# Optimization experiments

Measured on AMD Instinct MI355X. Metric: run time of the kernel, lower is better.

## Reference

```python
import jax, jax.numpy as jnp
import numpy as np

N = 8192      # atoms
B = 64        # molecules
E = 262144    # edges
S = 4         # species
NMAX = 8      # radial basis size
CUT = 5.0     # cutoff radius
AVG_ATOMS = 128.0
E_SCALE = 1.0
PS_DIM = (S * NMAX) ** 2 * 4  # l_max=3 -> 4 l channels -> 4096
H1, H2 = 1024, 1024
OUT = 1


def _sph_harm(u):
    # real spherical harmonics up to l=3, input unit vectors [E,3] -> [E,16]
    x, y, z = u[:, 0], u[:, 1], u[:, 2]
    x2, y2, z2 = x * x, y * y, z * z
    return jnp.stack([
        0.28209479 * jnp.ones_like(x),
        0.48860251 * y, 0.48860251 * z, 0.48860251 * x,
        1.09254843 * x * y, 1.09254843 * y * z, 0.31539157 * (3.0 * z2 - 1.0),
        1.09254843 * x * z, 0.54627422 * (x2 - y2),
        0.59004359 * y * (3.0 * x2 - y2), 2.89061144 * x * y * z,
        0.45704579 * y * (5.0 * z2 - 1.0), 0.37317633 * z * (5.0 * z2 - 3.0),
        0.45704579 * x * (5.0 * z2 - 1.0), 1.44530572 * z * (x2 - y2),
        0.59004359 * x * (x2 - 3.0 * y2),
    ], axis=-1)


def setup_inputs() -> dict:
    key = jax.random.key(0)
    ks = jax.random.split(key, 12)
    positions = jax.random.normal(ks[0], (N, 3), dtype=jnp.float32) * 1.5  # dense cloud so many pairs < CUT
    cells = jnp.tile(20.0 * jnp.eye(3, dtype=jnp.float32)[None], (B, 1, 1))
    numbers = jax.random.randint(ks[1], (N,), 0, S)
    edge_indices = jax.random.randint(ks[2], (2, E), 0, N)
    edge_offsets = jnp.zeros((E, 3), dtype=jnp.float32)
    batch = jnp.arange(N) // (N // B)
    gamma = 1.0 + 0.1 * jax.random.normal(ks[3], (PS_DIM,), dtype=jnp.float32)
    beta = 0.1 * jax.random.normal(ks[4], (PS_DIM,), dtype=jnp.float32)
    W_ps = jax.random.normal(ks[5], (PS_DIM, OUT), dtype=jnp.float32) / np.sqrt(PS_DIM)
    W1 = jax.random.normal(ks[6], (PS_DIM, H1), dtype=jnp.float32) / np.sqrt(PS_DIM)
    W2 = jax.random.normal(ks[7], (H1, H2), dtype=jnp.float32) / np.sqrt(H1)
    W3 = jax.random.normal(ks[8], (H2, OUT), dtype=jnp.float32) / np.sqrt(H2)
    W_comp = jax.random.normal(ks[9], (S, OUT), dtype=jnp.float32) / np.sqrt(S)
    return dict(positions=positions, cells=cells, numbers=numbers,
                edge_indices=edge_indices, edge_offsets=edge_offsets, batch=batch,
                gamma=gamma, beta=beta, W_ps=W_ps, W1=W1, W2=W2, W3=W3, W_comp=W_comp)


def reference(positions, cells, numbers, edge_indices, edge_offsets, batch,
              gamma, beta, W_ps, W1, W2, W3, W_comp):
    i, j = edge_indices[0], edge_indices[1]  # center, neighbor
    # periodic shift: fractional offsets through the cell of the center's molecule
    shift = jnp.einsum('ec,ecd->ed', edge_offsets, cells[batch[i]])
    rvec = positions[j] - positions[i] + shift                      # [E,3]
    r = jnp.sqrt(jnp.sum(rvec * rvec, axis=-1) + 1e-12)             # [E]
    u = rvec / r[:, None]
    fc = 0.5 * (jnp.cos(jnp.pi * jnp.minimum(r, CUT) / CUT) + 1.0) * (r < CUT)
    n = jnp.arange(1, NMAX + 1, dtype=positions.dtype)
    R = fc[:, None] * jnp.sin(jnp.pi * n[None, :] * r[:, None] / CUT) / r[:, None]  # [E,NMAX]
    Y = _sph_harm(u)                                                # [E,16]
    edge_feat = R[:, :, None] * Y[:, None, :]                       # [E,NMAX,16]
    # spherical expansion c[i, species(j), n, lm] via scatter-add
    seg = i * S + numbers[j]
    c = jax.ops.segment_sum(edge_feat, seg, num_segments=N * S)     # [N*S,NMAX,16]
    c = c.reshape(N, S * NMAX, 16)
    # power spectrum: contract over m within each l block
    bounds = [(0, 1), (1, 4), (4, 9), (9, 16)]
    p = [jnp.einsum('ixm,iym->ixy', c[:, :, s:e], c[:, :, s:e]) for s, e in bounds]
    ps = jnp.stack(p, axis=-1).reshape(N, PS_DIM)                   # [N,4096]
    # LayerNorm (eps=1e-5, affine)
    mu = jnp.mean(ps, axis=-1, keepdims=True)
    var = jnp.var(ps, axis=-1, keepdims=True)
    psn = (ps - mu) / jnp.sqrt(var + 1e-5) * gamma + beta
    # linear branch + MLP branch
    psl = psn @ W_ps                                                # [N,1]
    h = jax.nn.silu(psn @ W1)
    h = jax.nn.silu(h @ W2)
    psnn = h @ W3                                                   # [N,1]
    # pool atomic energies into per-molecule totals (index_add)
    energies = jax.ops.segment_sum(psl + psnn, batch, num_segments=B) / AVG_ATOMS
    # eval path: composition baseline
    comp = jax.ops.segment_sum(jax.nn.one_hot(numbers, S, dtype=psn.dtype), batch, num_segments=B)
    return energies * E_SCALE + comp @ W_comp                       # [B,1]
```

## Files before the change

### kernel.cpp

```cpp
#include <hip/hip_runtime.h>
#include <hip/hip_bf16.h>
#include <math.h>

#define N_ATOMS 8192
#define B_BATCH 64
#define E_EDGES 262144
#define S_SPEC 4
#define NMAX 8
#define PS_DIM 4096
#define H1_DIM 1024
#define CAP4 48
#define CUTR 5.0f
#define PI_F 3.14159265358979f

typedef __bf16 bf16;
typedef bf16 bf16x8 __attribute__((ext_vector_type(8)));
typedef float floatx4 __attribute__((ext_vector_type(4)));
typedef int intx8 __attribute__((ext_vector_type(8)));
typedef unsigned char u8;

__device__ __forceinline__ void g2lds16(const void* g, void* l) {
    __builtin_amdgcn_global_load_lds(
        (const __attribute__((address_space(1))) void*)g,
        (__attribute__((address_space(3))) void*)l, 16, 0, 0);
}

__device__ __forceinline__ int pk_fp8x4(float a, float b, float c, float d) {
    int lo = __builtin_amdgcn_cvt_pk_fp8_f32(a, b, 0, false);
    return __builtin_amdgcn_cvt_pk_fp8_f32(c, d, lo, true);
}

__global__ __launch_bounds__(256) void scatter_kernel(
    const float* __restrict__ pos, const float* __restrict__ cells,
    const int* __restrict__ numbers, const int* __restrict__ ei,
    const float* __restrict__ eo, const int* __restrict__ batch,
    int* __restrict__ cnt, float4* __restrict__ bucket)
{
    int e = blockIdx.x * 256 + threadIdx.x;
    int i = ei[e];
    int j = ei[E_EDGES + e];
    int b = batch[i];
    const float* cell = cells + b * 9;
    float o0 = eo[e * 3 + 0], o1 = eo[e * 3 + 1], o2 = eo[e * 3 + 2];
    float rv[3];
    #pragma unroll
    for (int d = 0; d < 3; ++d) {
        float shift = o0 * cell[0 * 3 + d] + o1 * cell[1 * 3 + d] + o2 * cell[2 * 3 + d];
        rv[d] = pos[j * 3 + d] - pos[i * 3 + d] + shift;
    }
    float r2 = rv[0] * rv[0] + rv[1] * rv[1] + rv[2] * rv[2] + 1e-12f;
    if (r2 >= CUTR * CUTR) return;
    float r = sqrtf(r2);
    float a1 = r * (PI_F / CUTR);
    int sp = numbers[j];
    int q = i * S_SPEC + sp;
    int slot = atomicAdd(&cnt[q], 1);
    if (slot < CAP4)
        bucket[q * CAP4 + slot] = make_float4(rv[0], rv[1], rv[2], a1);
}

__global__ __launch_bounds__(256) void transpose_convert2(
    const float* __restrict__ W1, u8* __restrict__ Wt1,
    const float* __restrict__ W2, u8* __restrict__ Wt2)
{
    const float* W; u8* Wt; int K; float scale; int bx;
    if (blockIdx.x < 128) { W = W1; Wt = Wt1; K = PS_DIM; scale = 64.0f; bx = blockIdx.x; }
    else                  { W = W2; Wt = Wt2; K = H1_DIM; scale = 32.0f; bx = blockIdx.x - 128; }
    const int Nc = H1_DIM;
    __shared__ float t[32][33];
    int k0 = bx * 32, n0 = blockIdx.y * 32;
    int tx = threadIdx.x & 31, ty = threadIdx.x >> 5;
    #pragma unroll
    for (int r = 0; r < 32; r += 8)
        t[ty + r][tx] = W[(size_t)(k0 + ty + r) * Nc + n0 + tx];
    __syncthreads();
    if (threadIdx.x < 64) {
        int nl = threadIdx.x >> 1, cc = threadIdx.x & 1;
        int n = n0 + nl;
        unsigned int w[4];
        #pragma unroll
        for (int g = 0; g < 4; ++g) {
            int kb = cc * 16 + g * 4;
            w[g] = (unsigned int)pk_fp8x4(
                t[kb + 0][nl] * scale, t[kb + 1][nl] * scale,
                t[kb + 2][nl] * scale, t[kb + 3][nl] * scale);
        }
        int gc = (k0 >> 4) + cc;
        int gcs = (gc & ~7) | ((gc & 7) ^ (n & 7));
        *(uint4*)(Wt + (size_t)n * K + (size_t)gcs * 16) = make_uint4(w[0], w[1], w[2], w[3]);
    }
}

__global__ __launch_bounds__(256) void accum_ps_kernel(
    const float4* __restrict__ bucket, const int* __restrict__ cnt,
    const float* __restrict__ gamma, const float* __restrict__ beta,
    const float* __restrict__ Wps, u8* __restrict__ psn, float* __restrict__ psl)
{
    __shared__ __align__(16) float cl[4][32 * 20];
    __shared__ __align__(16) u8 ps_s8[PS_DIM];
    __shared__ float red[8];
    __shared__ float red2[4];

    int t = threadIdx.x;
    int wv = t >> 6, lane = t & 63;
    int atom0 = blockIdx.x * 4;

    {
        int atom = atom0 + wv;
        int sp_l = lane >> 4;
        int nidx = (lane >> 1) & 7;
        float nf = (float)(nidx + 1);
        int par = lane & 1;

        int myCnt = cnt[atom * S_SPEC + sp_l];
        if (myCnt > CAP4) myCnt = CAP4;
        int m1 = max(myCnt, __shfl_xor(myCnt, 16));
        int mx = max(m1, __shfl_xor(m1, 32));

        const float4* q = bucket + (size_t)(atom * S_SPEC + sp_l) * CAP4;
        float acc[8] = {};
        #pragma unroll 2
        for (int e = 0; e < mx; ++e) {
            float4 d = q[e];
            bool valid = e < myCnt;
            float a1 = d.w;
            float inv_r = (PI_F / CUTR) * __frcp_rn(a1);
            float fc = 0.5f * __cosf(a1) + 0.5f;
            float rn = fc * inv_r * __sinf(nf * a1);
            rn = valid ? rn : 0.0f;

            float x = d.x * inv_r, y = d.y * inv_r, z = d.z * inv_r;
            float x2 = x * x, y2 = y * y, z2 = z * z;
            float Ys[8];
            if (par == 0) {
                Ys[0] = 0.28209479f;
                Ys[1] = 0.48860251f * y;
                Ys[2] = 0.48860251f * z;
                Ys[3] = 0.48860251f * x;
                Ys[4] = 1.09254843f * x * y;
                Ys[5] = 1.09254843f * y * z;
                Ys[6] = 0.31539157f * (3.0f * z2 - 1.0f);
                Ys[7] = 1.09254843f * x * z;
            } else {
                Ys[0] = 0.54627422f * (x2 - y2);
                Ys[1] = 0.59004359f * y * (3.0f * x2 - y2);
                Ys[2] = 2.89061144f * x * y * z;
                Ys[3] = 0.45704579f * y * (5.0f * z2 - 1.0f);
                Ys[4] = 0.37317633f * z * (5.0f * z2 - 3.0f);
                Ys[5] = 0.45704579f * x * (5.0f * z2 - 1.0f);
                Ys[6] = 1.44530572f * z * (x2 - y2);
                Ys[7] = 0.59004359f * x * (x2 - 3.0f * y2);
            }
            #pragma unroll
            for (int k = 0; k < 8; ++k) acc[k] += rn * Ys[k];
        }
        int X = sp_l * 8 + nidx;
        float* dst = &cl[wv][X * 20 + par * 8];
        *(float4*)(dst + 0) = make_float4(acc[0], acc[1], acc[2], acc[3]);
        *(float4*)(dst + 4) = make_float4(acc[4], acc[5], acc[6], acc[7]);
    }
    __syncthreads();

    for (int a = 0; a < 4; ++a) {
        int atom = atom0 + a;
        const float* cl_x = cl[a];

        int y = t & 31;
        int xb = t >> 5;
        float4 cya = *(const float4*)&cl_x[y * 20 + 0];
        float4 cyb = *(const float4*)&cl_x[y * 20 + 4];
        float4 cyc = *(const float4*)&cl_x[y * 20 + 8];
        float4 cyd = *(const float4*)&cl_x[y * 20 + 12];

        float ps[4][4];
        float sum = 0.0f, sumsq = 0.0f;
        #pragma unroll
        for (int q = 0; q < 4; ++q) {
            int x = xb + 8 * q;
            float4 xa = *(const float4*)&cl_x[x * 20 + 0];
            float4 xbv = *(const float4*)&cl_x[x * 20 + 4];
            float4 xc = *(const float4*)&cl_x[x * 20 + 8];
            float4 xd = *(const float4*)&cl_x[x * 20 + 12];
            float s0 = xa.x * cya.x;
            float s1 = xa.y * cya.y + xa.z * cya.z + xa.w * cya.w;
            float s2 = xbv.x * cyb.x + xbv.y * cyb.y + xbv.z * cyb.z + xbv.w * cyb.w
                     + xc.x * cyc.x;
            float s3 = xc.y * cyc.y + xc.z * cyc.z + xc.w * cyc.w
                     + xd.x * cyd.x + xd.y * cyd.y + xd.z * cyd.z + xd.w * cyd.w;
            ps[q][0] = s0; ps[q][1] = s1; ps[q][2] = s2; ps[q][3] = s3;
            sum += s0 + s1 + s2 + s3;
            sumsq += s0 * s0 + s1 * s1 + s2 * s2 + s3 * s3;
        }
        #pragma unroll
        for (int o = 32; o > 0; o >>= 1) {
            sum += __shfl_down(sum, o);
            sumsq += __shfl_down(sumsq, o);
        }
        if ((t & 63) == 0) { red[wv] = sum; red[4 + wv] = sumsq; }
        __syncthreads();
        float tot = red[0] + red[1] + red[2] + red[3];
        float totsq = red[4] + red[5] + red[6] + red[7];
        float mu = tot * (1.0f / PS_DIM);
        float var = totsq * (1.0f / PS_DIM) - mu * mu;
        float inv = rsqrtf(var + 1e-5f);

        float pacc = 0.0f;
        #pragma unroll
        for (int q = 0; q < 4; ++q) {
            int p = t + 256 * q;
            float4 g = *(const float4*)(gamma + p * 4);
            float4 bt = *(const float4*)(beta + p * 4);
            float4 w = *(const float4*)(Wps + p * 4);
            float v0 = (ps[q][0] - mu) * inv * g.x + bt.x;
            float v1 = (ps[q][1] - mu) * inv * g.y + bt.y;
            float v2 = (ps[q][2] - mu) * inv * g.z + bt.z;
            float v3 = (ps[q][3] - mu) * inv * g.w + bt.w;
            pacc += v0 * w.x + v1 * w.y + v2 * w.z + v3 * w.w;
            ((int*)ps_s8)[p] = pk_fp8x4(v0, v1, v2, v3);
        }
        __syncthreads();
        u8* rowp = psn + (size_t)atom * PS_DIM;
        int key = atom & 7;
        int gcs = (t & ~7) | ((t & 7) ^ key);
        *(uint4*)(rowp + (size_t)gcs * 16) = *(const uint4*)(ps_s8 + (size_t)t * 16);

        #pragma unroll
        for (int o = 32; o > 0; o >>= 1) pacc += __shfl_down(pacc, o);
        if ((t & 63) == 0) red2[wv] = pacc;
        __syncthreads();
        if (t == 0) psl[atom] = red2[0] + red2[1] + red2[2] + red2[3];
    }
}

__global__ __launch_bounds__(256) void gemm_f8_kernel(
    const u8* __restrict__ A, const u8* __restrict__ Bt,
    u8* __restrict__ H, int M, int Nc, int K, float invs)
{
    __shared__ __align__(16) char smem[65536];
    int tid = threadIdx.x;
    int bm = blockIdx.x, bn = blockIdx.y;
    int wave = tid >> 6, lane = tid & 63;
    int wm = (wave >> 1) * 64, wn = (wave & 1) * 64;
    int lm = lane & 15, quad = lane >> 4;

    floatx4 acc[4][4] = {};
    const int rowA0 = bm * 128, rowB0 = bn * 128;
    const size_t stride = (size_t)K;
    const char* Ab = (const char*)A + (size_t)rowA0 * stride;
    const char* Bb = (const char*)Bt + (size_t)rowB0 * stride;
    const int sA = 0x7F7F7F7F, sB = 0x7F7F7F7F;

    for (int k0 = 0; k0 < K; k0 += 256) {
        #pragma unroll
        for (int s = 0; s < 8; ++s) {
            int L = s * 256 + tid;
            int row = L >> 4, boff = (L & 15) * 16;
            int lbase = (s * 256 + wave * 64) * 16;
            g2lds16(Ab + (size_t)row * stride + k0 + boff, smem + lbase);
        }
        #pragma unroll
        for (int s = 0; s < 8; ++s) {
            int L = s * 256 + tid;
            int row = L >> 4, boff = (L & 15) * 16;
            int lbase = (s * 256 + wave * 64) * 16;
            g2lds16(Bb + (size_t)row * stride + k0 + boff, smem + 32768 + lbase);
        }
        __syncthreads();
        int key = lm & 7;
        int c0 = (2 * quad) ^ key, c1 = (2 * quad + 1) ^ key;
        #pragma unroll
        for (int h = 0; h < 2; ++h) {
            intx8 af[4], bfr[4];
            #pragma unroll
            for (int mi = 0; mi < 4; ++mi) {
                const char* base = smem + (wm + mi * 16 + lm) * 256 + h * 128;
                uint4 lo = *(const uint4*)(base + c0 * 16);
                uint4 hi = *(const uint4*)(base + c1 * 16);
                af[mi][0] = lo.x; af[mi][1] = lo.y; af[mi][2] = lo.z; af[mi][3] = lo.w;
                af[mi][4] = hi.x; af[mi][5] = hi.y; af[mi][6] = hi.z; af[mi][7] = hi.w;
            }
            #pragma unroll
            for (int ni = 0; ni < 4; ++ni) {
                const char* base = smem + 32768 + (wn + ni * 16 + lm) * 256 + h * 128;
                uint4 lo = *(const uint4*)(base + c0 * 16);
                uint4 hi = *(const uint4*)(base + c1 * 16);
                bfr[ni][0] = lo.x; bfr[ni][1] = lo.y; bfr[ni][2] = lo.z; bfr[ni][3] = lo.w;
                bfr[ni][4] = hi.x; bfr[ni][5] = hi.y; bfr[ni][6] = hi.z; bfr[ni][7] = hi.w;
            }
            #pragma unroll
            for (int mi = 0; mi < 4; ++mi)
                #pragma unroll
                for (int ni = 0; ni < 4; ++ni)
                    acc[mi][ni] = __builtin_amdgcn_mfma_scale_f32_16x16x128_f8f6f4(
                        af[mi], bfr[ni], acc[mi][ni], 0, 0, 0, sA, 0, sB);
        }
        __syncthreads();
    }

    u8* Cs8 = (u8*)smem;
    #pragma unroll
    for (int mi = 0; mi < 4; ++mi)
        #pragma unroll
        for (int ni = 0; ni < 4; ++ni)
            #pragma unroll
            for (int r = 0; r < 4; ++r) {
                int row = wm + mi * 16 + quad * 4 + r;
                int col = wn + ni * 16 + lm;
                float v = acc[mi][ni][r] * invs;
                v = v / (1.0f + __expf(-v));
                int pk = __builtin_amdgcn_cvt_pk_fp8_f32(v, 0.0f, 0, false);
                Cs8[row * 128 + col] = (u8)(pk & 0xFF);
            }
    __syncthreads();
    #pragma unroll
    for (int c2 = 0; c2 < 4; ++c2) {
        int L = c2 * 256 + tid;
        int row = L >> 3, cc = L & 7;
        int gcs = cc ^ (row & 7);
        *(uint4*)(H + (size_t)(rowA0 + row) * Nc + (size_t)(bn * 8 + gcs) * 16) =
            *(const uint4*)(Cs8 + (size_t)L * 16);
    }
}

__global__ __launch_bounds__(256) void gemm2_fused_kernel(
    const u8* __restrict__ A, const u8* __restrict__ Bt,
    const float* __restrict__ W3, float* __restrict__ nn_part,
    int Nc, int K, float invs)
{
    __shared__ __align__(16) char smem[65536];
    int tid = threadIdx.x;
    int bm = blockIdx.x, bn = blockIdx.y;
    int wave = tid >> 6, lane = tid & 63;
    int wm = (wave >> 1) * 64, wn = (wave & 1) * 64;
    int lm = lane & 15, quad = lane >> 4;

    floatx4 acc[4][4] = {};
    const int rowA0 = bm * 128, rowB0 = bn * 128;
    const size_t stride = (size_t)K;
    const char* Ab = (const char*)A + (size_t)rowA0 * stride;
    const char* Bb = (const char*)Bt + (size_t)rowB0 * stride;
    const int sA = 0x7F7F7F7F, sB = 0x7F7F7F7F;

    for (int k0 = 0; k0 < K; k0 += 256) {
        #pragma unroll
        for (int s = 0; s < 8; ++s) {
            int L = s * 256 + tid;
            int row = L >> 4, boff = (L & 15) * 16;
            int lbase = (s * 256 + wave * 64) * 16;
            g2lds16(Ab + (size_t)row * stride + k0 + boff, smem + lbase);
        }
        #pragma unroll
        for (int s = 0; s < 8; ++s) {
            int L = s * 256 + tid;
            int row = L >> 4, boff = (L & 15) * 16;
            int lbase = (s * 256 + wave * 64) * 16;
            g2lds16(Bb + (size_t)row * stride + k0 + boff, smem + 32768 + lbase);
        }
        __syncthreads();
        int key = lm & 7;
        int c0 = (2 * quad) ^ key, c1 = (2 * quad + 1) ^ key;
        #pragma unroll
        for (int h = 0; h < 2; ++h) {
            intx8 af[4], bfr[4];
            #pragma unroll
            for (int mi = 0; mi < 4; ++mi) {
                const char* base = smem + (wm + mi * 16 + lm) * 256 + h * 128;
                uint4 lo = *(const uint4*)(base + c0 * 16);
                uint4 hi = *(const uint4*)(base + c1 * 16);
                af[mi][0] = lo.x; af[mi][1] = lo.y; af[mi][2] = lo.z; af[mi][3] = lo.w;
                af[mi][4] = hi.x; af[mi][5] = hi.y; af[mi][6] = hi.z; af[mi][7] = hi.w;
            }
            #pragma unroll
            for (int ni = 0; ni < 4; ++ni) {
                const char* base = smem + 32768 + (wn + ni * 16 + lm) * 256 + h * 128;
                uint4 lo = *(const uint4*)(base + c0 * 16);
                uint4 hi = *(const uint4*)(base + c1 * 16);
                bfr[ni][0] = lo.x; bfr[ni][1] = lo.y; bfr[ni][2] = lo.z; bfr[ni][3] = lo.w;
                bfr[ni][4] = hi.x; bfr[ni][5] = hi.y; bfr[ni][6] = hi.z; bfr[ni][7] = hi.w;
            }
            #pragma unroll
            for (int mi = 0; mi < 4; ++mi)
                #pragma unroll
                for (int ni = 0; ni < 4; ++ni)
                    acc[mi][ni] = __builtin_amdgcn_mfma_scale_f32_16x16x128_f8f6f4(
                        af[mi], bfr[ni], acc[mi][ni], 0, 0, 0, sA, 0, sB);
        }
        __syncthreads();
    }

    float lt = 0.0f;
    #pragma unroll
    for (int ni = 0; ni < 4; ++ni) {
        float w3v = W3[bn * 128 + wn + ni * 16 + lm];
        #pragma unroll
        for (int mi = 0; mi < 4; ++mi)
            #pragma unroll
            for (int r = 0; r < 4; ++r) {
                float v = acc[mi][ni][r] * invs;
                v = v / (1.0f + __expf(-v));
                lt += v * w3v;
            }
    }
    #pragma unroll
    for (int o = 32; o > 0; o >>= 1) lt += __shfl_down(lt, o);
    float* wsum = (float*)smem;
    if (lane == 0) wsum[wave] = lt;
    __syncthreads();
    if (tid == 0)
        nn_part[bm * 8 + bn] = wsum[0] + wsum[1] + wsum[2] + wsum[3];
}

__global__ __launch_bounds__(128) void finalize_kernel(
    const float* __restrict__ psl, const int* __restrict__ numbers,
    const float* __restrict__ nn_part, const float* __restrict__ Wcomp,
    float* __restrict__ out)
{
    int b = blockIdx.x, t = threadIdx.x;
    __shared__ float sh[2];
    __shared__ int cnt4[S_SPEC];
    if (t < S_SPEC) cnt4[t] = 0;
    __syncthreads();
    int a = b * 128 + t;
    float e = psl[a];
    if (t < 8) e += nn_part[b * 8 + t];
    atomicAdd(&cnt4[numbers[a]], 1);
    #pragma unroll
    for (int o = 32; o > 0; o >>= 1) e += __shfl_down(e, o);
    if ((t & 63) == 0) sh[t >> 6] = e;
    __syncthreads();
    if (t == 0) {
        float r = (sh[0] + sh[1]) * (1.0f / 128.0f);
        #pragma unroll
        for (int s = 0; s < S_SPEC; ++s) r += (float)cnt4[s] * Wcomp[s];
        out[b] = r;
    }
}

extern "C" void kernel_launch(void* const* d_in, const int* in_sizes, int n_in,
                              void* d_out, int out_size, void* d_ws, size_t ws_size,
                              hipStream_t stream)
{
    const float* positions = (const float*)d_in[0];
    const float* cells     = (const float*)d_in[1];
    const int*   numbers   = (const int*)d_in[2];
    const int*   ei        = (const int*)d_in[3];
    const float* eo        = (const float*)d_in[4];
    const int*   batch     = (const int*)d_in[5];
    const float* gamma     = (const float*)d_in[6];
    const float* beta      = (const float*)d_in[7];
    const float* W_ps      = (const float*)d_in[8];
    const float* W1        = (const float*)d_in[9];
    const float* W2        = (const float*)d_in[10];
    const float* W3        = (const float*)d_in[11];
    const float* W_comp    = (const float*)d_in[12];
    float* out = (float*)d_out;

    char* ws = (char*)d_ws;
    float4* bucket = (float4*)ws;  ws += (size_t)N_ATOMS * S_SPEC * CAP4 * 16;
    u8*    psn  = (u8*)ws;     ws += (size_t)N_ATOMS * PS_DIM;
    u8*    h1   = (u8*)ws;     ws += (size_t)N_ATOMS * H1_DIM;
    u8*    Wt1  = (u8*)ws;     ws += (size_t)H1_DIM * PS_DIM;
    u8*    Wt2  = (u8*)ws;     ws += (size_t)H1_DIM * H1_DIM;
    float* psl  = (float*)ws;  ws += (size_t)N_ATOMS * 4;
    int*   cnt  = (int*)ws;    ws += (size_t)N_ATOMS * S_SPEC * 4;
    float* nn_part = (float*)ws; ws += (size_t)1024 * 4;

    hipMemsetAsync(cnt, 0, N_ATOMS * S_SPEC * sizeof(int), stream);

    scatter_kernel<<<E_EDGES / 256, 256, 0, stream>>>(
        positions, cells, numbers, ei, eo, batch, cnt, bucket);

    transpose_convert2<<<dim3(160, 32), 256, 0, stream>>>(W1, Wt1, W2, Wt2);

    accum_ps_kernel<<<N_ATOMS / 4, 256, 0, stream>>>(
        bucket, cnt, gamma, beta, W_ps, psn, psl);

    gemm_f8_kernel<<<dim3(N_ATOMS / 128, H1_DIM / 128), 256, 0, stream>>>(
        psn, Wt1, h1, N_ATOMS, H1_DIM, PS_DIM, 1.0f / 64.0f);
    gemm2_fused_kernel<<<dim3(N_ATOMS / 128, H1_DIM / 128), 256, 0, stream>>>(
        h1, Wt2, W3, nn_part, H1_DIM, H1_DIM, 1.0f / 32.0f);

    finalize_kernel<<<B_BATCH, 128, 0, stream>>>(psl, numbers, nn_part, W_comp, out);
}
```

Measured before the change: 198.3 us.

## Double-buffer FP8 GEMM K-tiles and write H directly via swapped MFMA operands

Both FP8 GEMM kernels now work on 128-wide K tiles held in two LDS buffers. The next tile's global-to-LDS loads are issued before the MFMAs on the current tile, so memory latency overlaps compute instead of waiting at each barrier. In the first GEMM the MFMA operands are swapped so each lane holds four consecutive output columns. Those four values are packed into one FP8 word and written straight to global memory in the swizzled layout, which removes the LDS staging pass and its extra barrier. The cost is an LDS wait and barrier on every (now smaller) K step, and 4-byte global stores in place of 16-byte ones.

```diff
diff --git a/kernel.cpp b/kernel.cpp
--- a/kernel.cpp
+++ b/kernel.cpp
@@ -250,75 +250,81 @@
     const char* Bb = (const char*)Bt + (size_t)rowB0 * stride;
     const int sA = 0x7F7F7F7F, sB = 0x7F7F7F7F;
 
-    for (int k0 = 0; k0 < K; k0 += 256) {
-        #pragma unroll
-        for (int s = 0; s < 8; ++s) {
-            int L = s * 256 + tid;
-            int row = L >> 4, boff = (L & 15) * 16;
-            int lbase = (s * 256 + wave * 64) * 16;
-            g2lds16(Ab + (size_t)row * stride + k0 + boff, smem + lbase);
-        }
-        #pragma unroll
-        for (int s = 0; s < 8; ++s) {
-            int L = s * 256 + tid;
-            int row = L >> 4, boff = (L & 15) * 16;
-            int lbase = (s * 256 + wave * 64) * 16;
-            g2lds16(Bb + (size_t)row * stride + k0 + boff, smem + 32768 + lbase);
-        }
-        __syncthreads();
-        int key = lm & 7;
-        int c0 = (2 * quad) ^ key, c1 = (2 * quad + 1) ^ key;
-        #pragma unroll
-        for (int h = 0; h < 2; ++h) {
-            intx8 af[4], bfr[4];
+    int srow = tid >> 3;
+    int sc = (tid & 7) * 16;
+
+    #pragma unroll
+    for (int s = 0; s < 4; ++s) {
+        int row = s * 32 + srow;
+        int lb = (s * 256 + wave * 64) * 16;
+        g2lds16(Ab + (size_t)row * stride + sc, smem + lb);
+        g2lds16(Bb + (size_t)row * stride + sc, smem + 16384 + lb);
+    }
+    asm volatile("s_waitcnt vmcnt(0)");
+    __syncthreads();
+
+    int key = lm & 7;
+    int c0 = (2 * quad) ^ key, c1 = (2 * quad + 1) ^ key;
+    const int nIter = K >> 7;
+    int cur = 0;
+
+    for (int t = 0; t < nIter; ++t) {
+        if (t + 1 < nIter) {
+            int k0 = (t + 1) << 7;
+            int nb = (cur ^ 1) * 32768;
             #pragma unroll
-            for (int mi = 0; mi < 4; ++mi) {
-                const char* base = smem + (wm + mi * 16 + lm) * 256 + h * 128;
-                uint4 lo = *(const uint4*)(base + c0 * 16);
-                uint4 hi = *(const uint4*)(base + c1 * 16);
-                af[mi][0] = lo.x; af[mi][1] = lo.y; af[mi][2] = lo.z; af[mi][3] = lo.w;
-                af[mi][4] = hi.x; af[mi][5] = hi.y; af[mi][6] = hi.z; af[mi][7] = hi.w;
+            for (int s = 0; s < 4; ++s) {
+                int row = s * 32 + srow;
+                int lb = nb + (s * 256 + wave * 64) * 16;
+                g2lds16(Ab + (size_t)row * stride + k0 + sc, smem + lb);
+                g2lds16(Bb + (size_t)row * stride + k0 + sc, smem + 16384 + lb);
             }
-            #pragma unroll
-            for (int ni = 0; ni < 4; ++ni) {
-                const char* base = smem + 32768 + (wn + ni * 16 + lm) * 256 + h * 128;
-                uint4 lo = *(const uint4*)(base + c0 * 16);
-                uint4 hi = *(const uint4*)(base + c1 * 16);
-                bfr[ni][0] = lo.x; bfr[ni][1] = lo.y; bfr[ni][2] = lo.z; bfr[ni][3] = lo.w;
-                bfr[ni][4] = hi.x; bfr[ni][5] = hi.y; bfr[ni][6] = hi.z; bfr[ni][7] = hi.w;
-            }
+        }
+        const char* baseA = smem + cur * 32768;
+        const char* baseB = baseA + 16384;
+        intx8 af[4], bfr[4];
+        #pragma unroll
+        for (int mi = 0; mi < 4; ++mi) {
+            const char* base = baseA + (wm + mi * 16 + lm) * 128;
+            uint4 lo = *(const uint4*)(base + c0 * 16);
+            uint4 hi = *(const uint4*)(base + c1 * 16);
+            af[mi][0] = lo.x; af[mi][1] = lo.y; af[mi][2] = lo.z; af[mi][3] = lo.w;
+            af[mi][4] = hi.x; af[mi][5] = hi.y; af[mi][6] = hi.z; af[mi][7] = hi.w;
+        }
+        #pragma unroll
+        for (int ni = 0; ni < 4; ++ni) {
+            const char* base = baseB + (wn + ni * 16 + lm) * 128;
+            uint4 lo = *(const uint4*)(base + c0 * 16);
+            uint4 hi = *(const uint4*)(base + c1 * 16);
+            bfr[ni][0] = lo.x; bfr[ni][1] = lo.y; bfr[ni][2] = lo.z; bfr[ni][3] = lo.w;
+            bfr[ni][4] = hi.x; bfr[ni][5] = hi.y; bfr[ni][6] = hi.z; bfr[ni][7] = hi.w;
+        }
+        #pragma unroll
+        for (int ni = 0; ni < 4; ++ni)
             #pragma unroll
             for (int mi = 0; mi < 4; ++mi)
-                #pragma unroll
-                for (int ni = 0; ni < 4; ++ni)
-                    acc[mi][ni] = __builtin_amdgcn_mfma_scale_f32_16x16x128_f8f6f4(
-                        af[mi], bfr[ni], acc[mi][ni], 0, 0, 0, sA, 0, sB);
-        }
+                acc[ni][mi] = __builtin_amdgcn_mfma_scale_f32_16x16x128_f8f6f4(
+                    bfr[ni], af[mi], acc[ni][mi], 0, 0, 0, sB, 0, sA);
+        asm volatile("s_waitcnt vmcnt(0)");
         __syncthreads();
-    }
-
-    u8* Cs8 = (u8*)smem;
-    #pragma unroll
-    for (int mi = 0; mi < 4; ++mi)
-        #pragma unroll
-        for (int ni = 0; ni < 4; ++ni)
-            #pragma unroll
-            for (int r = 0; r < 4; ++r) {
-                int row = wm + mi * 16 + quad * 4 + r;
-                int col = wn + ni * 16 + lm;
-                float v = acc[mi][ni][r] * invs;
-                v = v / (1.0f + __expf(-v));
-                int pk = __builtin_amdgcn_cvt_pk_fp8_f32(v, 0.0f, 0, false);
-                Cs8[row * 128 + col] = (u8)(pk & 0xFF);
-            }
-    __syncthreads();
-    #pragma unroll
-    for (int c2 = 0; c2 < 4; ++c2) {
-        int L = c2 * 256 + tid;
-        int row = L >> 3, cc = L & 7;
-        int gcs = cc ^ (row & 7);
-        *(uint4*)(H + (size_t)(rowA0 + row) * Nc + (size_t)(bn * 8 + gcs) * 16) =
-            *(const uint4*)(Cs8 + (size_t)L * 16);
+        cur ^= 1;
+    }
+
+    #pragma unroll
+    for (int ni = 0; ni < 4; ++ni) {
+        int cc = (wn >> 4) + ni;
+        #pragma unroll
+        for (int mi = 0; mi < 4; ++mi) {
+            int atom = rowA0 + wm + mi * 16 + lm;
+            float v0 = acc[ni][mi][0] * invs; v0 = v0 / (1.0f + __expf(-v0));
+            float v1 = acc[ni][mi][1] * invs; v1 = v1 / (1.0f + __expf(-v1));
+            float v2 = acc[ni][mi][2] * invs; v2 = v2 / (1.0f + __expf(-v2));
+            float v3 = acc[ni][mi][3] * invs; v3 = v3 / (1.0f + __expf(-v3));
+            unsigned int pk = (unsigned int)pk_fp8x4(v0, v1, v2, v3);
+            size_t addr = (size_t)atom * Nc + bn * 128
+                        + (size_t)((cc ^ (atom & 7)) * 16) + quad * 4;
+            *(unsigned int*)(H + addr) = pk;
+        }
     }
 }
 
@@ -341,51 +347,64 @@
     const char* Bb = (const char*)Bt + (size_t)rowB0 * stride;
     const int sA = 0x7F7F7F7F, sB = 0x7F7F7F7F;
 
-    for (int k0 = 0; k0 < K; k0 += 256) {
-        #pragma unroll
-        for (int s = 0; s < 8; ++s) {
-            int L = s * 256 + tid;
-            int row = L >> 4, boff = (L & 15) * 16;
-            int lbase = (s * 256 + wave * 64) * 16;
-            g2lds16(Ab + (size_t)row * stride + k0 + boff, smem + lbase);
-        }
-        #pragma unroll
-        for (int s = 0; s < 8; ++s) {
-            int L = s * 256 + tid;
-            int row = L >> 4, boff = (L & 15) * 16;
-            int lbase = (s * 256 + wave * 64) * 16;
-            g2lds16(Bb + (size_t)row * stride + k0 + boff, smem + 32768 + lbase);
-        }
+    int srow = tid >> 3;
+    int sc = (tid & 7) * 16;
+
+    #pragma unroll
+    for (int s = 0; s < 4; ++s) {
+        int row = s * 32 + srow;
+        int lb = (s * 256 + wave * 64) * 16;
+        g2lds16(Ab + (size_t)row * stride + sc, smem + lb);
+        g2lds16(Bb + (size_t)row * stride + sc, smem + 16384 + lb);
+    }
+    asm volatile("s_waitcnt vmcnt(0)");
+    __syncthreads();
+
+    int key = lm & 7;
+    int c0 = (2 * quad) ^ key, c1 = (2 * quad + 1) ^ key;
+    const int nIter = K >> 7;
+    int cur = 0;
+
+    for (int t = 0; t < nIter; ++t) {
+        if (t + 1 < nIter) {
+            int k0 = (t + 1) << 7;
+            int nb = (cur ^ 1) * 32768;
+            #pragma unroll
+            for (int s = 0; s < 4; ++s) {
+                int row = s * 32 + srow;
+                int lb = nb + (s * 256 + wave * 64) * 16;
+                g2lds16(Ab + (size_t)row * stride + k0 + sc, smem + lb);
+                g2lds16(Bb + (size_t)row * stride + k0 + sc, smem + 16384 + lb);
+            }
+        }
+        const char* baseA = smem + cur * 32768;
+        const char* baseB = baseA + 16384;
+        intx8 af[4], bfr[4];
+        #pragma unroll
+        for (int mi = 0; mi < 4; ++mi) {
+            const char* base = baseA + (wm + mi * 16 + lm) * 128;
+            uint4 lo = *(const uint4*)(base + c0 * 16);
+            uint4 hi = *(const uint4*)(base + c1 * 16);
+            af[mi][0] = lo.x; af[mi][1] = lo.y; af[mi][2] = lo.z; af[mi][3] = lo.w;
+            af[mi][4] = hi.x; af[mi][5] = hi.y; af[mi][6] = hi.z; af[mi][7] = hi.w;
+        }
+        #pragma unroll
+        for (int ni = 0; ni < 4; ++ni) {
+            const char* base = baseB + (wn + ni * 16 + lm) * 128;
+            uint4 lo = *(const uint4*)(base + c0 * 16);
+            uint4 hi = *(const uint4*)(base + c1 * 16);
+            bfr[ni][0] = lo.x; bfr[ni][1] = lo.y; bfr[ni][2] = lo.z; bfr[ni][3] = lo.w;
+            bfr[ni][4] = hi.x; bfr[ni][5] = hi.y; bfr[ni][6] = hi.z; bfr[ni][7] = hi.w;
+        }
+        #pragma unroll
+        for (int mi = 0; mi < 4; ++mi)
+            #pragma unroll
+            for (int ni = 0; ni < 4; ++ni)
+                acc[mi][ni] = __builtin_amdgcn_mfma_scale_f32_16x16x128_f8f6f4(
+                    af[mi], bfr[ni], acc[mi][ni], 0, 0, 0, sA, 0, sB);
+        asm volatile("s_waitcnt vmcnt(0)");
         __syncthreads();
-        int key = lm & 7;
-        int c0 = (2 * quad) ^ key, c1 = (2 * quad + 1) ^ key;
-        #pragma unroll
-        for (int h = 0; h < 2; ++h) {
-            intx8 af[4], bfr[4];
-            #pragma unroll
-            for (int mi = 0; mi < 4; ++mi) {
-                const char* base = smem + (wm + mi * 16 + lm) * 256 + h * 128;
-                uint4 lo = *(const uint4*)(base + c0 * 16);
-                uint4 hi = *(const uint4*)(base + c1 * 16);
-                af[mi][0] = lo.x; af[mi][1] = lo.y; af[mi][2] = lo.z; af[mi][3] = lo.w;
-                af[mi][4] = hi.x; af[mi][5] = hi.y; af[mi][6] = hi.z; af[mi][7] = hi.w;
-            }
-            #pragma unroll
-            for (int ni = 0; ni < 4; ++ni) {
-                const char* base = smem + 32768 + (wn + ni * 16 + lm) * 256 + h * 128;
-                uint4 lo = *(const uint4*)(base + c0 * 16);
-                uint4 hi = *(const uint4*)(base + c1 * 16);
-                bfr[ni][0] = lo.x; bfr[ni][1] = lo.y; bfr[ni][2] = lo.z; bfr[ni][3] = lo.w;
-                bfr[ni][4] = hi.x; bfr[ni][5] = hi.y; bfr[ni][6] = hi.z; bfr[ni][7] = hi.w;
-            }
-            #pragma unroll
-            for (int mi = 0; mi < 4; ++mi)
-                #pragma unroll
-                for (int ni = 0; ni < 4; ++ni)
-                    acc[mi][ni] = __builtin_amdgcn_mfma_scale_f32_16x16x128_f8f6f4(
-                        af[mi], bfr[ni], acc[mi][ni], 0, 0, 0, sA, 0, sB);
-        }
-        __syncthreads();
+        cur ^= 1;
     }
 
     float lt = 0.0f;
```

New measurement: 203.8 us. +2.8%, slower.

## Prepack FP8 weights into MFMA fragment layout and double-buffer activation tiles

Applied to the files above, without the earlier changes.

The weight transpose kernel now writes FP8 weights in a 16-row by 128-byte fragment-blocked layout. This lets both GEMM kernels load B fragments straight from global memory into registers instead of staging them through LDS. The A tile is double-buffered in LDS, with the next k-step prefetched while MFMAs run, which removes one barrier per iteration. The first GEMM swaps operands to produce transposed accumulators and writes packed 4-byte FP8 outputs directly, dropping the LDS epilogue staging. The tradeoff is more global load traffic per wave for B, which now relies on cache hits instead of LDS reuse.

```diff
diff --git a/kernel.cpp b/kernel.cpp
--- a/kernel.cpp
+++ b/kernel.cpp
@@ -85,9 +85,12 @@
                 t[kb + 0][nl] * scale, t[kb + 1][nl] * scale,
                 t[kb + 2][nl] * scale, t[kb + 3][nl] * scale);
         }
-        int gc = (k0 >> 4) + cc;
-        int gcs = (gc & ~7) | ((gc & 7) ^ (n & 7));
-        *(uint4*)(Wt + (size_t)n * K + (size_t)gcs * 16) = make_uint4(w[0], w[1], w[2], w[3]);
+        int kk = k0 + cc * 16;
+        int kseg = kk >> 7;
+        int koff = kk & 127;
+        size_t addr = ((size_t)(n >> 4) * (K >> 7) + kseg) * 2048
+                    + (size_t)(n & 15) * 128 + koff;
+        *(uint4*)(Wt + addr) = make_uint4(w[0], w[1], w[2], w[3]);
     }
 }
 
@@ -244,81 +247,109 @@
     int lm = lane & 15, quad = lane >> 4;
 
     floatx4 acc[4][4] = {};
-    const int rowA0 = bm * 128, rowB0 = bn * 128;
+    const int rowA0 = bm * 128;
     const size_t stride = (size_t)K;
     const char* Ab = (const char*)A + (size_t)rowA0 * stride;
-    const char* Bb = (const char*)Bt + (size_t)rowB0 * stride;
     const int sA = 0x7F7F7F7F, sB = 0x7F7F7F7F;
 
-    for (int k0 = 0; k0 < K; k0 += 256) {
-        #pragma unroll
-        for (int s = 0; s < 8; ++s) {
-            int L = s * 256 + tid;
-            int row = L >> 4, boff = (L & 15) * 16;
-            int lbase = (s * 256 + wave * 64) * 16;
-            g2lds16(Ab + (size_t)row * stride + k0 + boff, smem + lbase);
-        }
-        #pragma unroll
-        for (int s = 0; s < 8; ++s) {
-            int L = s * 256 + tid;
-            int row = L >> 4, boff = (L & 15) * 16;
-            int lbase = (s * 256 + wave * 64) * 16;
-            g2lds16(Bb + (size_t)row * stride + k0 + boff, smem + 32768 + lbase);
-        }
+    const int ksegs = K >> 7;
+    const u8* Bw = Bt + ((size_t)(bn * 8 + (wn >> 4)) * ksegs) * 2048
+                 + (size_t)lm * 128 + quad * 32;
+
+    int key = lm & 7;
+    int c0 = (2 * quad) ^ key, c1 = (2 * quad + 1) ^ key;
+
+    #pragma unroll
+    for (int s = 0; s < 8; ++s) {
+        int L = s * 256 + tid;
+        int row = L >> 4, boff = (L & 15) * 16;
+        g2lds16(Ab + (size_t)row * stride + boff, smem + (s * 256 + wave * 64) * 16);
+    }
+    __syncthreads();
+
+    const int nIter = K >> 8;
+    int cur = 0;
+
+    for (int t = 0; t < nIter; ++t) {
+        if (t + 1 < nIter) {
+            int kn = (t + 1) << 8;
+            int nb = (cur ^ 1) * 32768;
+            #pragma unroll
+            for (int s = 0; s < 8; ++s) {
+                int L = s * 256 + tid;
+                int row = L >> 4, boff = (L & 15) * 16;
+                g2lds16(Ab + (size_t)row * stride + kn + boff,
+                        smem + nb + (s * 256 + wave * 64) * 16);
+            }
+        }
+        const char* baseA = smem + cur * 32768;
+        int seg0 = t * 2;
+
+        intx8 bfr0[4], bfr1[4];
+        #pragma unroll
+        for (int ni = 0; ni < 4; ++ni) {
+            const u8* p = Bw + ((size_t)ni * ksegs + seg0) * 2048;
+            uint4 lo = *(const uint4*)p;
+            uint4 hi = *(const uint4*)(p + 16);
+            bfr0[ni][0] = lo.x; bfr0[ni][1] = lo.y; bfr0[ni][2] = lo.z; bfr0[ni][3] = lo.w;
+            bfr0[ni][4] = hi.x; bfr0[ni][5] = hi.y; bfr0[ni][6] = hi.z; bfr0[ni][7] = hi.w;
+        }
+        intx8 af[4];
+        #pragma unroll
+        for (int mi = 0; mi < 4; ++mi) {
+            const char* base = baseA + (wm + mi * 16 + lm) * 256;
+            uint4 lo = *(const uint4*)(base + c0 * 16);
+            uint4 hi = *(const uint4*)(base + c1 * 16);
+            af[mi][0] = lo.x; af[mi][1] = lo.y; af[mi][2] = lo.z; af[mi][3] = lo.w;
+            af[mi][4] = hi.x; af[mi][5] = hi.y; af[mi][6] = hi.z; af[mi][7] = hi.w;
+        }
+        #pragma unroll
+        for (int ni = 0; ni < 4; ++ni) {
+            const u8* p = Bw + ((size_t)ni * ksegs + seg0 + 1) * 2048;
+            uint4 lo = *(const uint4*)p;
+            uint4 hi = *(const uint4*)(p + 16);
+            bfr1[ni][0] = lo.x; bfr1[ni][1] = lo.y; bfr1[ni][2] = lo.z; bfr1[ni][3] = lo.w;
+            bfr1[ni][4] = hi.x; bfr1[ni][5] = hi.y; bfr1[ni][6] = hi.z; bfr1[ni][7] = hi.w;
+        }
+        #pragma unroll
+        for (int ni = 0; ni < 4; ++ni)
+            #pragma unroll
+            for (int mi = 0; mi < 4; ++mi)
+                acc[ni][mi] = __builtin_amdgcn_mfma_scale_f32_16x16x128_f8f6f4(
+                    bfr0[ni], af[mi], acc[ni][mi], 0, 0, 0, sB, 0, sA);
+        #pragma unroll
+        for (int mi = 0; mi < 4; ++mi) {
+            const char* base = baseA + (wm + mi * 16 + lm) * 256 + 128;
+            uint4 lo = *(const uint4*)(base + c0 * 16);
+            uint4 hi = *(const uint4*)(base + c1 * 16);
+            af[mi][0] = lo.x; af[mi][1] = lo.y; af[mi][2] = lo.z; af[mi][3] = lo.w;
+            af[mi][4] = hi.x; af[mi][5] = hi.y; af[mi][6] = hi.z; af[mi][7] = hi.w;
+        }
+        #pragma unroll
+        for (int ni = 0; ni < 4; ++ni)
+            #pragma unroll
+            for (int mi = 0; mi < 4; ++mi)
+                acc[ni][mi] = __builtin_amdgcn_mfma_scale_f32_16x16x128_f8f6f4(
+                    bfr1[ni], af[mi], acc[ni][mi], 0, 0, 0, sB, 0, sA);
         __syncthreads();
-        int key = lm & 7;
-        int c0 = (2 * quad) ^ key, c1 = (2 * quad + 1) ^ key;
-        #pragma unroll
-        for (int h = 0; h < 2; ++h) {
-            intx8 af[4], bfr[4];
-            #pragma unroll
-            for (int mi = 0; mi < 4; ++mi) {
-                const char* base = smem + (wm + mi * 16 + lm) * 256 + h * 128;
-                uint4 lo = *(const uint4*)(base + c0 * 16);
-                uint4 hi = *(const uint4*)(base + c1 * 16);
-                af[mi][0] = lo.x; af[mi][1] = lo.y; af[mi][2] = lo.z; af[mi][3] = lo.w;
-                af[mi][4] = hi.x; af[mi][5] = hi.y; af[mi][6] = hi.z; af[mi][7] = hi.w;
-            }
-            #pragma unroll
-            for (int ni = 0; ni < 4; ++ni) {
-                const char* base = smem + 32768 + (wn + ni * 16 + lm) * 256 + h * 128;
-                uint4 lo = *(const uint4*)(base + c0 * 16);
-                uint4 hi = *(const uint4*)(base + c1 * 16);
-                bfr[ni][0] = lo.x; bfr[ni][1] = lo.y; bfr[ni][2] = lo.z; bfr[ni][3] = lo.w;
-                bfr[ni][4] = hi.x; bfr[ni][5] = hi.y; bfr[ni][6] = hi.z; bfr[ni][7] = hi.w;
-            }
-            #pragma unroll
-            for (int mi = 0; mi < 4; ++mi)
-                #pragma unroll
-                for (int ni = 0; ni < 4; ++ni)
-                    acc[mi][ni] = __builtin_amdgcn_mfma_scale_f32_16x16x128_f8f6f4(
-                        af[mi], bfr[ni], acc[mi][ni], 0, 0, 0, sA, 0, sB);
-        }
-        __syncthreads();
-    }
-
-    u8* Cs8 = (u8*)smem;
-    #pragma unroll
-    for (int mi = 0; mi < 4; ++mi)
-        #pragma unroll
-        for (int ni = 0; ni < 4; ++ni)
-            #pragma unroll
-            for (int r = 0; r < 4; ++r) {
-                int row = wm + mi * 16 + quad * 4 + r;
-                int col = wn + ni * 16 + lm;
-                float v = acc[mi][ni][r] * invs;
-                v = v / (1.0f + __expf(-v));
-                int pk = __builtin_amdgcn_cvt_pk_fp8_f32(v, 0.0f, 0, false);
-                Cs8[row * 128 + col] = (u8)(pk & 0xFF);
-            }
-    __syncthreads();
-    #pragma unroll
-    for (int c2 = 0; c2 < 4; ++c2) {
-        int L = c2 * 256 + tid;
-        int row = L >> 3, cc = L & 7;
-        int gcs = cc ^ (row & 7);
-        *(uint4*)(H + (size_t)(rowA0 + row) * Nc + (size_t)(bn * 8 + gcs) * 16) =
-            *(const uint4*)(Cs8 + (size_t)L * 16);
+        cur ^= 1;
+    }
+
+    #pragma unroll
+    for (int ni = 0; ni < 4; ++ni) {
+        int cc = (wn >> 4) + ni;
+        #pragma unroll
+        for (int mi = 0; mi < 4; ++mi) {
+            int atom = rowA0 + wm + mi * 16 + lm;
+            float v0 = acc[ni][mi][0] * invs; v0 = v0 / (1.0f + __expf(-v0));
+            float v1 = acc[ni][mi][1] * invs; v1 = v1 / (1.0f + __expf(-v1));
+            float v2 = acc[ni][mi][2] * invs; v2 = v2 / (1.0f + __expf(-v2));
+            float v3 = acc[ni][mi][3] * invs; v3 = v3 / (1.0f + __expf(-v3));
+            unsigned int pk = (unsigned int)pk_fp8x4(v0, v1, v2, v3);
+            size_t addr = (size_t)atom * Nc + bn * 128
+                        + (size_t)((cc ^ (atom & 7)) * 16) + quad * 4;
+            *(unsigned int*)(H + addr) = pk;
+        }
     }
 }
 
@@ -335,57 +366,92 @@
     int lm = lane & 15, quad = lane >> 4;
 
     floatx4 acc[4][4] = {};
-    const int rowA0 = bm * 128, rowB0 = bn * 128;
+    const int rowA0 = bm * 128;
     const size_t stride = (size_t)K;
     const char* Ab = (const char*)A + (size_t)rowA0 * stride;
-    const char* Bb = (const char*)Bt + (size_t)rowB0 * stride;
     const int sA = 0x7F7F7F7F, sB = 0x7F7F7F7F;
 
-    for (int k0 = 0; k0 < K; k0 += 256) {
-        #pragma unroll
-        for (int s = 0; s < 8; ++s) {
-            int L = s * 256 + tid;
-            int row = L >> 4, boff = (L & 15) * 16;
-            int lbase = (s * 256 + wave * 64) * 16;
-            g2lds16(Ab + (size_t)row * stride + k0 + boff, smem + lbase);
-        }
-        #pragma unroll
-        for (int s = 0; s < 8; ++s) {
-            int L = s * 256 + tid;
-            int row = L >> 4, boff = (L & 15) * 16;
-            int lbase = (s * 256 + wave * 64) * 16;
-            g2lds16(Bb + (size_t)row * stride + k0 + boff, smem + 32768 + lbase);
-        }
+    const int ksegs = K >> 7;
+    const u8* Bw = Bt + ((size_t)(bn * 8 + (wn >> 4)) * ksegs) * 2048
+                 + (size_t)lm * 128 + quad * 32;
+
+    int key = lm & 7;
+    int c0 = (2 * quad) ^ key, c1 = (2 * quad + 1) ^ key;
+
+    #pragma unroll
+    for (int s = 0; s < 8; ++s) {
+        int L = s * 256 + tid;
+        int row = L >> 4, boff = (L & 15) * 16;
+        g2lds16(Ab + (size_t)row * stride + boff, smem + (s * 256 + wave * 64) * 16);
+    }
+    __syncthreads();
+
+    const int nIter = K >> 8;
+    int cur = 0;
+
+    for (int t = 0; t < nIter; ++t) {
+        if (t + 1 < nIter) {
+            int kn = (t + 1) << 8;
+            int nb = (cur ^ 1) * 32768;
+            #pragma unroll
+            for (int s = 0; s < 8; ++s) {
+                int L = s * 256 + tid;
+                int row = L >> 4, boff = (L & 15) * 16;
+                g2lds16(Ab + (size_t)row * stride + kn + boff,
+                        smem + nb + (s * 256 + wave * 64) * 16);
+            }
+        }
+        const char* baseA = smem + cur * 32768;
+        int seg0 = t * 2;
+
+        intx8 bfr0[4], bfr1[4];
+        #pragma unroll
+        for (int ni = 0; ni < 4; ++ni) {
+            const u8* p = Bw + ((size_t)ni * ksegs + seg0) * 2048;
+            uint4 lo = *(const uint4*)p;
+            uint4 hi = *(const uint4*)(p + 16);
+            bfr0[ni][0] = lo.x; bfr0[ni][1] = lo.y; bfr0[ni][2] = lo.z; bfr0[ni][3] = lo.w;
+            bfr0[ni][4] = hi.x; bfr0[ni][5] = hi.y; bfr0[ni][6] = hi.z; bfr0[ni][7] = hi.w;
+        }
+        intx8 af[4];
+        #pragma unroll
+        for (int mi = 0; mi < 4; ++mi) {
+            const char* base = baseA + (wm + mi * 16 + lm) * 256;
+            uint4 lo = *(const uint4*)(base + c0 * 16);
+            uint4 hi = *(const uint4*)(base + c1 * 16);
+            af[mi][0] = lo.x; af[mi][1] = lo.y; af[mi][2] = lo.z; af[mi][3] = lo.w;
+            af[mi][4] = hi.x; af[mi][5] = hi.y; af[mi][6] = hi.z; af[mi][7] = hi.w;
+        }
+        #pragma unroll
+        for (int ni = 0; ni < 4; ++ni) {
+            const u8* p = Bw + ((size_t)ni * ksegs + seg0 + 1) * 2048;
+            uint4 lo = *(const uint4*)p;
+            uint4 hi = *(const uint4*)(p + 16);
+            bfr1[ni][0] = lo.x; bfr1[ni][1] = lo.y; bfr1[ni][2] = lo.z; bfr1[ni][3] = lo.w;
+            bfr1[ni][4] = hi.x; bfr1[ni][5] = hi.y; bfr1[ni][6] = hi.z; bfr1[ni][7] = hi.w;
+        }
+        #pragma unroll
+        for (int mi = 0; mi < 4; ++mi)
+            #pragma unroll
+            for (int ni = 0; ni < 4; ++ni)
+                acc[mi][ni] = __builtin_amdgcn_mfma_scale_f32_16x16x128_f8f6f4(
+                    af[mi], bfr0[ni], acc[mi][ni], 0, 0, 0, sA, 0, sB);
+        #pragma unroll
+        for (int mi = 0; mi < 4; ++mi) {
+            const char* base = baseA + (wm + mi * 16 + lm) * 256 + 128;
+            uint4 lo = *(const uint4*)(base + c0 * 16);
+            uint4 hi = *(const uint4*)(base + c1 * 16);
+            af[mi][0] = lo.x; af[mi][1] = lo.y; af[mi][2] = lo.z; af[mi][3] = lo.w;
+            af[mi][4] = hi.x; af[mi][5] = hi.y; af[mi][6] = hi.z; af[mi][7] = hi.w;
+        }
+        #pragma unroll
+        for (int mi = 0; mi < 4; ++mi)
+            #pragma unroll
+            for (int ni = 0; ni < 4; ++ni)
+                acc[mi][ni] = __builtin_amdgcn_mfma_scale_f32_16x16x128_f8f6f4(
+                    af[mi], bfr1[ni], acc[mi][ni], 0, 0, 0, sA, 0, sB);
         __syncthreads();
-        int key = lm & 7;
-        int c0 = (2 * quad) ^ key, c1 = (2 * quad + 1) ^ key;
-        #pragma unroll
-        for (int h = 0; h < 2; ++h) {
-            intx8 af[4], bfr[4];
-            #pragma unroll
-            for (int mi = 0; mi < 4; ++mi) {
-                const char* base = smem + (wm + mi * 16 + lm) * 256 + h * 128;
-                uint4 lo = *(const uint4*)(base + c0 * 16);
-                uint4 hi = *(const uint4*)(base + c1 * 16);
-                af[mi][0] = lo.x; af[mi][1] = lo.y; af[mi][2] = lo.z; af[mi][3] = lo.w;
-                af[mi][4] = hi.x; af[mi][5] = hi.y; af[mi][6] = hi.z; af[mi][7] = hi.w;
-            }
-            #pragma unroll
-            for (int ni = 0; ni < 4; ++ni) {
-                const char* base = smem + 32768 + (wn + ni * 16 + lm) * 256 + h * 128;
-                uint4 lo = *(const uint4*)(base + c0 * 16);
-                uint4 hi = *(const uint4*)(base + c1 * 16);
-                bfr[ni][0] = lo.x; bfr[ni][1] = lo.y; bfr[ni][2] = lo.z; bfr[ni][3] = lo.w;
-                bfr[ni][4] = hi.x; bfr[ni][5] = hi.y; bfr[ni][6] = hi.z; bfr[ni][7] = hi.w;
-            }
-            #pragma unroll
-            for (int mi = 0; mi < 4; ++mi)
-                #pragma unroll
-                for (int ni = 0; ni < 4; ++ni)
-                    acc[mi][ni] = __builtin_amdgcn_mfma_scale_f32_16x16x128_f8f6f4(
-                        af[mi], bfr[ni], acc[mi][ni], 0, 0, 0, sA, 0, sB);
-        }
-        __syncthreads();
+        cur ^= 1;
     }
 
     float lt = 0.0f;
```

Measured after the change: 239.3 us. +20.7%, slower.

## Exploit power-spectrum symmetry and fold LayerNorm affine into W1 to shrink GEMM K

Applied to the files above, without the earlier changes.

The power spectrum is symmetric in (x,y), so only the upper-triangular 528 pairs times 4 l-channels are kept. Padded to 2304, this shrinks the first GEMM's K dimension and the psn buffer from 4096. The LayerNorm gamma is folded into a combined W1 (summing the mirrored rows), and beta@W1 becomes a bias added in the GEMM epilogue, so accum_ps now stores the normalized z values. This cuts GEMM1 work and psn traffic by almost half. In exchange, weight prep gains a scalar-loop index decode and a bias atomicAdd, and fp8 quantization now applies to z and the folded weights.

```diff
diff --git a/kernel.cpp b/kernel.cpp
--- a/kernel.cpp
+++ b/kernel.cpp
@@ -8,6 +8,7 @@
 #define S_SPEC 4
 #define NMAX 8
 #define PS_DIM 4096
+#define PS_K 2304
 #define H1_DIM 1024
 #define CAP4 48
 #define CUTR 5.0f
@@ -59,20 +60,73 @@
         bucket[q * CAP4 + slot] = make_float4(rv[0], rv[1], rv[2], a1);
 }
 
-__global__ __launch_bounds__(256) void transpose_convert2(
-    const float* __restrict__ W1, u8* __restrict__ Wt1,
+__global__ __launch_bounds__(256) void build_w1f_kernel(
+    const float* __restrict__ W1, const float* __restrict__ gamma,
+    const float* __restrict__ beta, u8* __restrict__ Wt1, float* __restrict__ b1)
+{
+    __shared__ float tbuf[32][33];
+    __shared__ float bred[8][32];
+    int k0 = blockIdx.x * 32, n0 = blockIdx.y * 32;
+    int tx = threadIdx.x & 31, ty = threadIdx.x >> 5;
+    float bacc = 0.0f;
+    for (int r = 0; r < 32; r += 8) {
+        int kk = ty + r;
+        int kp = k0 + kk;
+        int u = kp >> 2, lb = kp & 3;
+        float val = 0.0f;
+        if (u < 528) {
+            int x = 0;
+            while ((x + 1) * (64 - x) / 2 <= u) ++x;
+            int y = x + (u - x * (65 - x) / 2);
+            int p1 = x * 128 + y * 4 + lb;
+            float w1v = W1[(size_t)p1 * H1_DIM + n0 + tx];
+            val = gamma[p1] * w1v;
+            bacc += beta[p1] * w1v;
+            if (x < y) {
+                int p2 = y * 128 + x * 4 + lb;
+                float w2v = W1[(size_t)p2 * H1_DIM + n0 + tx];
+                val += gamma[p2] * w2v;
+                bacc += beta[p2] * w2v;
+            }
+        }
+        tbuf[kk][tx] = val;
+    }
+    bred[ty][tx] = bacc;
+    __syncthreads();
+    if (ty == 0) {
+        float s = 0.0f;
+        #pragma unroll
+        for (int i = 0; i < 8; ++i) s += bred[i][tx];
+        atomicAdd(&b1[n0 + tx], s);
+    }
+    if (threadIdx.x < 64) {
+        int nl = threadIdx.x >> 1, cc = threadIdx.x & 1;
+        int n = n0 + nl;
+        unsigned int w[4];
+        #pragma unroll
+        for (int g = 0; g < 4; ++g) {
+            int kb = cc * 16 + g * 4;
+            w[g] = (unsigned int)pk_fp8x4(
+                tbuf[kb + 0][nl] * 64.0f, tbuf[kb + 1][nl] * 64.0f,
+                tbuf[kb + 2][nl] * 64.0f, tbuf[kb + 3][nl] * 64.0f);
+        }
+        int gc = (k0 >> 4) + cc;
+        int gcs = (gc & ~7) | ((gc & 7) ^ (n & 7));
+        *(uint4*)(Wt1 + (size_t)n * PS_K + (size_t)gcs * 16) = make_uint4(w[0], w[1], w[2], w[3]);
+    }
+}
+
+__global__ __launch_bounds__(256) void transpose_w2_kernel(
     const float* __restrict__ W2, u8* __restrict__ Wt2)
 {
-    const float* W; u8* Wt; int K; float scale; int bx;
-    if (blockIdx.x < 128) { W = W1; Wt = Wt1; K = PS_DIM; scale = 64.0f; bx = blockIdx.x; }
-    else                  { W = W2; Wt = Wt2; K = H1_DIM; scale = 32.0f; bx = blockIdx.x - 128; }
-    const int Nc = H1_DIM;
+    const int K = H1_DIM, Nc = H1_DIM;
+    const float scale = 32.0f;
     __shared__ float t[32][33];
-    int k0 = bx * 32, n0 = blockIdx.y * 32;
+    int k0 = blockIdx.x * 32, n0 = blockIdx.y * 32;
     int tx = threadIdx.x & 31, ty = threadIdx.x >> 5;
     #pragma unroll
     for (int r = 0; r < 32; r += 8)
-        t[ty + r][tx] = W[(size_t)(k0 + ty + r) * Nc + n0 + tx];
+        t[ty + r][tx] = W2[(size_t)(k0 + ty + r) * Nc + n0 + tx];
     __syncthreads();
     if (threadIdx.x < 64) {
         int nl = threadIdx.x >> 1, cc = threadIdx.x & 1;
@@ -87,7 +141,7 @@
         }
         int gc = (k0 >> 4) + cc;
         int gcs = (gc & ~7) | ((gc & 7) ^ (n & 7));
-        *(uint4*)(Wt + (size_t)n * K + (size_t)gcs * 16) = make_uint4(w[0], w[1], w[2], w[3]);
+        *(uint4*)(Wt2 + (size_t)n * K + (size_t)gcs * 16) = make_uint4(w[0], w[1], w[2], w[3]);
     }
 }
 
@@ -97,7 +151,7 @@
     const float* __restrict__ Wps, u8* __restrict__ psn, float* __restrict__ psl)
 {
     __shared__ __align__(16) float cl[4][32 * 20];
-    __shared__ __align__(16) u8 ps_s8[PS_DIM];
+    __shared__ __align__(16) u8 ps_s8[PS_K];
     __shared__ float red[8];
     __shared__ float red2[4];
 
@@ -159,6 +213,7 @@
         *(float4*)(dst + 0) = make_float4(acc[0], acc[1], acc[2], acc[3]);
         *(float4*)(dst + 4) = make_float4(acc[4], acc[5], acc[6], acc[7]);
     }
+    if (t < 48) ((int*)ps_s8)[528 + t] = 0;
     __syncthreads();
 
     for (int a = 0; a < 4; ++a) {
@@ -211,18 +266,27 @@
             float4 g = *(const float4*)(gamma + p * 4);
             float4 bt = *(const float4*)(beta + p * 4);
             float4 w = *(const float4*)(Wps + p * 4);
-            float v0 = (ps[q][0] - mu) * inv * g.x + bt.x;
-            float v1 = (ps[q][1] - mu) * inv * g.y + bt.y;
-            float v2 = (ps[q][2] - mu) * inv * g.z + bt.z;
-            float v3 = (ps[q][3] - mu) * inv * g.w + bt.w;
+            float z0 = (ps[q][0] - mu) * inv;
+            float z1 = (ps[q][1] - mu) * inv;
+            float z2 = (ps[q][2] - mu) * inv;
+            float z3 = (ps[q][3] - mu) * inv;
+            float v0 = z0 * g.x + bt.x;
+            float v1 = z1 * g.y + bt.y;
+            float v2 = z2 * g.z + bt.z;
+            float v3 = z3 * g.w + bt.w;
             pacc += v0 * w.x + v1 * w.y + v2 * w.z + v3 * w.w;
-            ((int*)ps_s8)[p] = pk_fp8x4(v0, v1, v2, v3);
-        }
-        __syncthreads();
-        u8* rowp = psn + (size_t)atom * PS_DIM;
-        int key = atom & 7;
-        int gcs = (t & ~7) | ((t & 7) ^ key);
-        *(uint4*)(rowp + (size_t)gcs * 16) = *(const uint4*)(ps_s8 + (size_t)t * 16);
+            int x = p >> 5, yy = p & 31;
+            if (x <= yy) {
+                int u = x * (65 - x) / 2 + (yy - x);
+                ((int*)ps_s8)[u] = pk_fp8x4(z0, z1, z2, z3);
+            }
+        }
+        __syncthreads();
+        u8* rowp = psn + (size_t)atom * PS_K;
+        if (t < PS_K / 16) {
+            int gcs = (t & ~7) | ((t & 7) ^ (atom & 7));
+            *(uint4*)(rowp + (size_t)gcs * 16) = *(const uint4*)(ps_s8 + (size_t)t * 16);
+        }
 
         #pragma unroll
         for (int o = 32; o > 0; o >>= 1) pacc += __shfl_down(pacc, o);
@@ -234,7 +298,8 @@
 
 __global__ __launch_bounds__(256) void gemm_f8_kernel(
     const u8* __restrict__ A, const u8* __restrict__ Bt,
-    u8* __restrict__ H, int M, int Nc, int K, float invs)
+    u8* __restrict__ H, const float* __restrict__ b1,
+    int M, int Nc, int K, float invs)
 {
     __shared__ __align__(16) char smem[65536];
     int tid = threadIdx.x;
@@ -301,16 +366,18 @@
     #pragma unroll
     for (int mi = 0; mi < 4; ++mi)
         #pragma unroll
-        for (int ni = 0; ni < 4; ++ni)
+        for (int ni = 0; ni < 4; ++ni) {
+            float bv = b1[bn * 128 + wn + ni * 16 + lm];
             #pragma unroll
             for (int r = 0; r < 4; ++r) {
                 int row = wm + mi * 16 + quad * 4 + r;
                 int col = wn + ni * 16 + lm;
-                float v = acc[mi][ni][r] * invs;
+                float v = acc[mi][ni][r] * invs + bv;
                 v = v / (1.0f + __expf(-v));
                 int pk = __builtin_amdgcn_cvt_pk_fp8_f32(v, 0.0f, 0, false);
                 Cs8[row * 128 + col] = (u8)(pk & 0xFF);
             }
+        }
     __syncthreads();
     #pragma unroll
     for (int c2 = 0; c2 < 4; ++c2) {
@@ -457,26 +524,30 @@
 
     char* ws = (char*)d_ws;
     float4* bucket = (float4*)ws;  ws += (size_t)N_ATOMS * S_SPEC * CAP4 * 16;
-    u8*    psn  = (u8*)ws;     ws += (size_t)N_ATOMS * PS_DIM;
+    u8*    psn  = (u8*)ws;     ws += (size_t)N_ATOMS * PS_K;
     u8*    h1   = (u8*)ws;     ws += (size_t)N_ATOMS * H1_DIM;
-    u8*    Wt1  = (u8*)ws;     ws += (size_t)H1_DIM * PS_DIM;
+    u8*    Wt1  = (u8*)ws;     ws += (size_t)H1_DIM * PS_K;
     u8*    Wt2  = (u8*)ws;     ws += (size_t)H1_DIM * H1_DIM;
     float* psl  = (float*)ws;  ws += (size_t)N_ATOMS * 4;
     int*   cnt  = (int*)ws;    ws += (size_t)N_ATOMS * S_SPEC * 4;
     float* nn_part = (float*)ws; ws += (size_t)1024 * 4;
+    float* b1   = (float*)ws;  ws += (size_t)H1_DIM * 4;
 
     hipMemsetAsync(cnt, 0, N_ATOMS * S_SPEC * sizeof(int), stream);
+    hipMemsetAsync(b1, 0, H1_DIM * sizeof(float), stream);
 
     scatter_kernel<<<E_EDGES / 256, 256, 0, stream>>>(
         positions, cells, numbers, ei, eo, batch, cnt, bucket);
 
-    transpose_convert2<<<dim3(160, 32), 256, 0, stream>>>(W1, Wt1, W2, Wt2);
+    build_w1f_kernel<<<dim3(PS_K / 32, 32), 256, 0, stream>>>(
+        W1, gamma, beta, Wt1, b1);
+    transpose_w2_kernel<<<dim3(32, 32), 256, 0, stream>>>(W2, Wt2);
 
     accum_ps_kernel<<<N_ATOMS / 4, 256, 0, stream>>>(
         bucket, cnt, gamma, beta, W_ps, psn, psl);
 
     gemm_f8_kernel<<<dim3(N_ATOMS / 128, H1_DIM / 128), 256, 0, stream>>>(
-        psn, Wt1, h1, N_ATOMS, H1_DIM, PS_DIM, 1.0f / 64.0f);
+        psn, Wt1, h1, b1, N_ATOMS, H1_DIM, PS_K, 1.0f / 64.0f);
     gemm2_fused_kernel<<<dim3(N_ATOMS / 128, H1_DIM / 128), 256, 0, stream>>>(
         h1, Wt2, W3, nn_part, H1_DIM, H1_DIM, 1.0f / 32.0f);
 
```

After: 198.5 us. No clear change (+0.1%).
